# Kernel optimization log

Hardware: AMD Instinct MI355X
Metric: run time of the kernel (lower is better)

The kernel has to match this reference:

```python
import jax, jax.numpy as jnp
import numpy as np

DIM = 2048
N_HEADS = 32
N_KV_HEADS = 8
HEAD_DIM = DIM // N_HEADS
B, T = 2, 2048


def setup_inputs() -> dict:
    key = jax.random.key(0)
    ks = jax.random.split(key, 5)
    std = 0.02
    return {
        "x": jax.random.normal(ks[0], (B, T, DIM), dtype=jnp.float32),
        "wq": jax.random.normal(ks[1], (DIM, DIM), dtype=jnp.float32) * std,
        "wk": jax.random.normal(ks[2], (N_KV_HEADS * HEAD_DIM, DIM), dtype=jnp.float32) * std,
        "wv": jax.random.normal(ks[3], (N_KV_HEADS * HEAD_DIM, DIM), dtype=jnp.float32) * std,
        "wo": jax.random.normal(ks[4], (DIM, DIM), dtype=jnp.float32) * std,
    }


def _rope_tables(seq_len, head_dim, dtype):
    inv_freq = 1.0 / (10000.0 ** (jnp.arange(0, head_dim, 2, dtype=jnp.float32) / head_dim))
    t = jnp.arange(seq_len, dtype=jnp.float32)
    freqs = jnp.einsum("i,j->ij", t, inv_freq)          # [T, hd/2]
    emb = jnp.concatenate([freqs, freqs], axis=-1)       # [T, hd]
    return jnp.cos(emb).astype(dtype), jnp.sin(emb).astype(dtype)


def _rotate_half(x):
    h = x.shape[-1] // 2
    return jnp.concatenate([-x[..., h:], x[..., :h]], axis=-1)


def reference(x, wq, wk, wv, wo):
    Bc, Tc, C = x.shape
    q = (x @ wq.T).reshape(Bc, Tc, N_HEADS, HEAD_DIM).transpose(0, 2, 1, 3)      # [B,H,T,hd]
    k = (x @ wk.T).reshape(Bc, Tc, N_KV_HEADS, HEAD_DIM).transpose(0, 2, 1, 3)   # [B,Hk,T,hd]
    v = (x @ wv.T).reshape(Bc, Tc, N_KV_HEADS, HEAD_DIM).transpose(0, 2, 1, 3)

    cos, sin = _rope_tables(Tc, HEAD_DIM, x.dtype)  # [T,hd] broadcast over B,H
    q = q * cos + _rotate_half(q) * sin
    k = k * cos + _rotate_half(k) * sin

    rep = N_HEADS // N_KV_HEADS
    k = jnp.repeat(k, rep, axis=1)  # [B,H,T,hd]
    v = jnp.repeat(v, rep, axis=1)

    scale = 1.0 / np.sqrt(HEAD_DIM)
    scores = jnp.einsum("bhqd,bhkd->bhqk", q, k) * scale   # [B,H,T,T]
    causal = jnp.triu(jnp.ones((Tc, Tc), dtype=bool), k=1)
    scores = jnp.where(causal, jnp.asarray(-jnp.inf, scores.dtype), scores)
    attn = jax.nn.softmax(scores, axis=-1)
    out = jnp.einsum("bhqk,bhkd->bhqd", attn, v)           # [B,H,T,hd]
    out = out.transpose(0, 2, 1, 3).reshape(Bc, Tc, C)
    return out @ wo.T
```

## Files before the change

kernel.cpp:

```cpp
#include <hip/hip_runtime.h>


typedef unsigned short u16;
typedef __attribute__((ext_vector_type(8))) short bf16x8;
typedef __attribute__((ext_vector_type(4))) float f32x4;
typedef __attribute__((ext_vector_type(4))) unsigned short u16x4;

constexpr int T_SEQ = 2048;
constexpr int DIMC  = 2048;
constexpr int NHEAD = 32;
constexpr int HDIM  = 64;
constexpr int KVDIM = 512;
constexpr int BATCH = 2;

__device__ __forceinline__ u16 f2bf(float f) {
    union { float f; unsigned int i; } v; v.f = f;
    unsigned int r = v.i + 0x7FFFu + ((v.i >> 16) & 1u);
    return (u16)(r >> 16);
}
__device__ __forceinline__ u16 f2bf_trunc(float f) {
    union { float f; unsigned int i; } v; v.f = f;
    return (u16)(v.i >> 16);
}

typedef __attribute__((address_space(1))) unsigned int as1_uint;
typedef __attribute__((address_space(3))) unsigned int as3_uint;
__device__ __forceinline__ void glds16(const u16* g, u16* l) {
    __builtin_amdgcn_global_load_lds((as1_uint*)(u16*)g, (as3_uint*)l, 16, 0, 0);
}

__global__ __launch_bounds__(256) void cvt5(const float* __restrict__ x,
                                            const float* __restrict__ wq,
                                            const float* __restrict__ wk,
                                            const float* __restrict__ wv,
                                            const float* __restrict__ wo,
                                            u16* __restrict__ xb,  u16* __restrict__ wqb,
                                            u16* __restrict__ wkb, u16* __restrict__ wvb,
                                            u16* __restrict__ wob) {
    constexpr int E0 = BATCH * T_SEQ * DIMC;
    constexpr int E1 = E0 + DIMC * DIMC;
    constexpr int E2 = E1 + KVDIM * DIMC;
    constexpr int E3 = E2 + KVDIM * DIMC;
    constexpr int E4 = E3 + DIMC * DIMC;
    for (int i = (blockIdx.x * 256 + threadIdx.x) * 4; i < E4; i += gridDim.x * 1024) {
        const float* s; u16* d; int off;
        if (i < E0)      { s = x;  d = xb;  off = 0;  }
        else if (i < E1) { s = wq; d = wqb; off = E0; }
        else if (i < E2) { s = wk; d = wkb; off = E1; }
        else if (i < E3) { s = wv; d = wvb; off = E2; }
        else             { s = wo; d = wob; off = E3; }
        f32x4 v = *(const f32x4*)(s + (i - off));
        u16x4 o;
        #pragma unroll
        for (int e = 0; e < 4; ++e) o[e] = f2bf(v[e]);
        *(u16x4*)(d + (i - off)) = o;
    }
}

template <bool OUTF32>
__device__ __forceinline__ void gemm_core(const u16* __restrict__ A,
                                          const u16* __restrict__ W,
                                          void* __restrict__ Cv,
                                          int rowBase, int colBase,
                                          int N, int K, bool rope) {
    __shared__ __align__(16) u16 As[2 * 128 * 32];
    __shared__ __align__(16) u16 Bs[2 * 128 * 32];

    const int tid  = threadIdx.x;
    const int lane = tid & 63;
    const int w    = tid >> 6;
    const int quad = lane >> 4;
    const int ln   = lane & 15;
    const int wm = (w >> 1) * 64;
    const int wn = (w & 1) * 64;

    f32x4 acc[4][4] = {};

    const int srow = lane >> 2;
    const int scol = (lane & 3) * 8;
    const u16* aC0 = A + (size_t)(rowBase + w * 16 + srow) * K + scol;
    const u16* aC1 = A + (size_t)(rowBase + (w + 4) * 16 + srow) * K + scol;
    const u16* bC0 = W + (size_t)(colBase + w * 16 + srow) * K + scol;
    const u16* bC1 = W + (size_t)(colBase + (w + 4) * 16 + srow) * K + scol;
    u16* asl0 = As + w * 512;
    u16* asl1 = As + (w + 4) * 512;
    u16* bsl0 = Bs + w * 512;
    u16* bsl1 = Bs + (w + 4) * 512;

    for (int kk = 0; kk < K; kk += 64) {
        __syncthreads();
        glds16(aC0 + kk, asl0);
        glds16(aC1 + kk, asl1);
        glds16(bC0 + kk, bsl0);
        glds16(bC1 + kk, bsl1);
        glds16(aC0 + kk + 32, asl0 + 4096);
        glds16(aC1 + kk + 32, asl1 + 4096);
        glds16(bC0 + kk + 32, bsl0 + 4096);
        glds16(bC1 + kk + 32, bsl1 + 4096);
        __syncthreads();

        #pragma unroll
        for (int hp = 0; hp < 2; ++hp) {
            const u16* Ap = As + hp * 4096;
            const u16* Bp = Bs + hp * 4096;
            bf16x8 bw[4];
            #pragma unroll
            for (int j = 0; j < 4; ++j)
                bw[j] = *(const bf16x8*)(Bp + (wn + j * 16 + ln) * 32 + quad * 8);
            #pragma unroll
            for (int i = 0; i < 4; ++i) {
                bf16x8 af = *(const bf16x8*)(Ap + (wm + i * 16 + ln) * 32 + quad * 8);
                #pragma unroll
                for (int j = 0; j < 4; ++j)
                    acc[i][j] = __builtin_amdgcn_mfma_f32_16x16x32_bf16(af, bw[j], acc[i][j], 0, 0, 0);
            }
        }
    }

    if (rope) {
        #pragma unroll
        for (int j = 0; j < 2; ++j) {
            const int d = j * 16 + ln;
            const float invrev = exp2f(-(float)d * (13.287712379549449f / 32.0f))
                                 * 0.15915494309189535f;
            #pragma unroll
            for (int i = 0; i < 4; ++i) {
                #pragma unroll
                for (int r = 0; r < 4; ++r) {
                    const int t = (rowBase + wm + i * 16 + quad * 4 + r) & (T_SEQ - 1);
                    float rev = (float)t * invrev;
                    float fr = rev - floorf(rev);
                    float sn = __builtin_amdgcn_sinf(fr);
                    float cs = __builtin_amdgcn_cosf(fr);
                    float a0 = acc[i][j][r], a2 = acc[i][j + 2][r];
                    acc[i][j][r]     = a0 * cs - a2 * sn;
                    acc[i][j + 2][r] = a2 * cs + a0 * sn;
                }
            }
        }
    }

    #pragma unroll
    for (int i = 0; i < 4; ++i) {
        int mrow = rowBase + wm + i * 16 + quad * 4;
        #pragma unroll
        for (int j = 0; j < 4; ++j) {
            int n = colBase + wn + j * 16 + ln;
            #pragma unroll
            for (int r = 0; r < 4; ++r) {
                if constexpr (OUTF32)
                    ((float*)Cv)[(size_t)(mrow + r) * N + n] = acc[i][j][r];
                else
                    ((u16*)Cv)[(size_t)(mrow + r) * N + n] = f2bf(acc[i][j][r]);
            }
        }
    }
}

__global__ __launch_bounds__(256, 4) void qkv_gemm(const u16* __restrict__ xb,
                                                   const u16* __restrict__ wqb,
                                                   const u16* __restrict__ wkb,
                                                   const u16* __restrict__ wvb,
                                                   u16* __restrict__ Qb,
                                                   u16* __restrict__ Kb,
                                                   u16* __restrict__ Vb) {
    const int nb = blockIdx.x;
    const int rowBase = blockIdx.y * 128;
    const u16* W; u16* C; int colBase, N; bool rope;
    if (nb < 16)      { W = wqb; C = Qb; colBase = nb * 128;        N = DIMC;  rope = true; }
    else if (nb < 20) { W = wkb; C = Kb; colBase = (nb - 16) * 128; N = KVDIM; rope = true; }
    else              { W = wvb; C = Vb; colBase = (nb - 20) * 128; N = KVDIM; rope = false; }
    gemm_core<false>(xb, W, C, rowBase, colBase, N, DIMC, rope);
}

__global__ __launch_bounds__(256, 4) void gemm_out64(const u16* __restrict__ A,
                                                     const u16* __restrict__ W,
                                                     float* __restrict__ C) {
    __shared__ __align__(16) u16 As[2 * 128 * 32];
    __shared__ __align__(16) u16 Bs[2 * 64 * 32];

    const int tid  = threadIdx.x;
    const int lane = tid & 63;
    const int w    = tid >> 6;
    const int quad = lane >> 4;
    const int ln   = lane & 15;
    const int rowBase = blockIdx.y * 128;
    const int colBase = blockIdx.x * 64;
    const int wm = w * 32;
    constexpr int K = DIMC, N = DIMC;

    f32x4 acc[2][4] = {};

    const int srow = lane >> 2;
    const int scol = (lane & 3) * 8;
    const u16* aC0 = A + (size_t)(rowBase + w * 16 + srow) * K + scol;
    const u16* aC1 = A + (size_t)(rowBase + (w + 4) * 16 + srow) * K + scol;
    const u16* bC  = W + (size_t)(colBase + w * 16 + srow) * K + scol;
    u16* asl0 = As + w * 512;
    u16* asl1 = As + (w + 4) * 512;
    u16* bsl  = Bs + w * 512;

    for (int kk = 0; kk < K; kk += 64) {
        __syncthreads();
        glds16(aC0 + kk, asl0);
        glds16(aC1 + kk, asl1);
        glds16(bC  + kk, bsl);
        glds16(aC0 + kk + 32, asl0 + 4096);
        glds16(aC1 + kk + 32, asl1 + 4096);
        glds16(bC  + kk + 32, bsl + 2048);
        __syncthreads();

        #pragma unroll
        for (int hp = 0; hp < 2; ++hp) {
            const u16* Ap = As + hp * 4096;
            const u16* Bp = Bs + hp * 2048;
            bf16x8 bw[4];
            #pragma unroll
            for (int j = 0; j < 4; ++j)
                bw[j] = *(const bf16x8*)(Bp + (j * 16 + ln) * 32 + quad * 8);
            #pragma unroll
            for (int i = 0; i < 2; ++i) {
                bf16x8 af = *(const bf16x8*)(Ap + (wm + i * 16 + ln) * 32 + quad * 8);
                #pragma unroll
                for (int j = 0; j < 4; ++j)
                    acc[i][j] = __builtin_amdgcn_mfma_f32_16x16x32_bf16(af, bw[j], acc[i][j], 0, 0, 0);
            }
        }
    }

    #pragma unroll
    for (int i = 0; i < 2; ++i) {
        int mrow = rowBase + wm + i * 16 + quad * 4;
        #pragma unroll
        for (int j = 0; j < 4; ++j) {
            int n = colBase + j * 16 + ln;
            #pragma unroll
            for (int r = 0; r < 4; ++r)
                C[(size_t)(mrow + r) * N + n] = acc[i][j][r];
        }
    }
}

__global__ __launch_bounds__(256) void transpose_v(const u16* __restrict__ V,
                                                   u16* __restrict__ Vt) {
    __shared__ __align__(16) u16 tile[32][33];
    const int x = threadIdx.x & 31;
    const int y = threadIdx.x >> 5;
    const int tok0 = blockIdx.y * 32;
    const int c0   = blockIdx.x * 32;
    #pragma unroll
    for (int yy = 0; yy < 32; yy += 8)
        tile[y + yy][x] = V[(size_t)(tok0 + y + yy) * KVDIM + c0 + x];
    __syncthreads();
    const int b  = tok0 >> 11;
    const int t0 = tok0 & (T_SEQ - 1);
    #pragma unroll
    for (int yy = 0; yy < 32; yy += 8)
        Vt[(size_t)(b * KVDIM + c0 + y + yy) * T_SEQ + t0 + x] = tile[x][y + yy];
}

__global__ __launch_bounds__(256) void attn(const u16* __restrict__ Q,
                                            const u16* __restrict__ Kx,
                                            const u16* __restrict__ Vt,
                                            u16* __restrict__ O) {
    __shared__ __align__(16) u16 Ks[64][72];
    __shared__ __align__(16) u16 Vs[64][72];
    __shared__ __align__(16) u16 Ps[4][16][72];

    const int tid  = threadIdx.x;
    const int lane = tid & 63;
    const int w    = tid >> 6;
    const int quad = lane >> 4;
    const int ln   = lane & 15;
    const int h    = blockIdx.y;
    const int b    = blockIdx.z;
    const int kvh  = h >> 2;

    const int srow = tid >> 2;
    const int scol = (tid & 3) * 16;
    const u16* kbase = Kx + (size_t)(b * T_SEQ + srow) * KVDIM + kvh * HDIM + scol;
    const u16* vbase = Vt + (size_t)(b * KVDIM + kvh * HDIM + srow) * T_SEQ;

    const float K1 = 0.125f * 1.4426950408889634f;
    const float K2 = 8.0f * 1.4426950408889634f;

    #pragma unroll
    for (int phase = 0; phase < 2; ++phase) {
        const int qt = phase ? (31 - (int)blockIdx.x) : (int)blockIdx.x;
        const int qr0 = qt * 64 + w * 16;

        const u16* qp = Q + (size_t)(b * T_SEQ + qr0 + ln) * DIMC + h * HDIM + quad * 8;
        const bf16x8 aq0 = *(const bf16x8*)qp;
        const bf16x8 aq1 = *(const bf16x8*)(qp + 32);

        f32x4 o[4] = {};
        float lpart[4] = {};

        for (int kt = 0; kt <= qt; ++kt) {
            const int k0 = kt * 64;
            __syncthreads();
            *(bf16x8*)&Ks[srow][scol]     = *(const bf16x8*)(kbase + (size_t)k0 * KVDIM);
            *(bf16x8*)&Ks[srow][scol + 8] = *(const bf16x8*)(kbase + (size_t)k0 * KVDIM + 8);
            *(bf16x8*)&Vs[srow][scol]     = *(const bf16x8*)(vbase + k0 + scol);
            *(bf16x8*)&Vs[srow][scol + 8] = *(const bf16x8*)(vbase + k0 + scol + 8);
            __syncthreads();

            f32x4 s[4];
            #pragma unroll
            for (int st = 0; st < 4; ++st) {
                f32x4 z = {};
                s[st] = __builtin_amdgcn_mfma_f32_16x16x32_bf16(
                            aq0, *(const bf16x8*)&Ks[st * 16 + ln][quad * 8], z, 0, 0, 0);
                s[st] = __builtin_amdgcn_mfma_f32_16x16x32_bf16(
                            aq1, *(const bf16x8*)&Ks[st * 16 + ln][32 + quad * 8], s[st], 0, 0, 0);
            }

            if (kt != qt) {
                #pragma unroll
                for (int r = 0; r < 4; ++r) {
                    float e[4], rs = 0.0f;
                    #pragma unroll
                    for (int st = 0; st < 4; ++st) {
                        e[st] = exp2f(fmaf(s[st][r], K1, -K2));
                        rs += e[st];
                    }
                    lpart[r] += rs;
                    #pragma unroll
                    for (int st = 0; st < 4; ++st)
                        Ps[w][quad * 4 + r][st * 16 + ln] = f2bf_trunc(e[st]);
                }
            } else {
                #pragma unroll
                for (int r = 0; r < 4; ++r) {
                    const int thr = w * 16 + quad * 4 + r;
                    float e[4], rs = 0.0f;
                    #pragma unroll
                    for (int st = 0; st < 4; ++st) {
                        bool masked = (st * 16 + ln > thr);
                        e[st] = masked ? 0.0f : exp2f(fmaf(s[st][r], K1, -K2));
                        rs += e[st];
                    }
                    lpart[r] += rs;
                    #pragma unroll
                    for (int st = 0; st < 4; ++st)
                        Ps[w][quad * 4 + r][st * 16 + ln] = f2bf_trunc(e[st]);
                }
            }
            __asm__ __volatile__("s_waitcnt lgkmcnt(0)" ::: "memory");

            bf16x8 pa0 = *(const bf16x8*)&Ps[w][ln][quad * 8];
            bf16x8 pa1 = *(const bf16x8*)&Ps[w][ln][32 + quad * 8];
            #pragma unroll
            for (int t = 0; t < 4; ++t) {
                o[t] = __builtin_amdgcn_mfma_f32_16x16x32_bf16(
                           pa0, *(const bf16x8*)&Vs[t * 16 + ln][quad * 8], o[t], 0, 0, 0);
                o[t] = __builtin_amdgcn_mfma_f32_16x16x32_bf16(
                           pa1, *(const bf16x8*)&Vs[t * 16 + ln][32 + quad * 8], o[t], 0, 0, 0);
            }
        }

        #pragma unroll
        for (int r = 0; r < 4; ++r) {
            float rs = lpart[r];
            rs += __shfl_xor(rs, 1);
            rs += __shfl_xor(rs, 2);
            rs += __shfl_xor(rs, 4);
            rs += __shfl_xor(rs, 8);
            float inv = 1.0f / rs;
            size_t obase = (size_t)(b * T_SEQ + qr0 + quad * 4 + r) * DIMC + h * HDIM;
            #pragma unroll
            for (int t = 0; t < 4; ++t)
                O[obase + t * 16 + ln] = f2bf(o[t][r] * inv);
        }
    }
}

extern "C" void kernel_launch(void* const* d_in, const int* in_sizes, int n_in,
                              void* d_out, int out_size, void* d_ws, size_t ws_size,
                              hipStream_t stream) {
    const float* x  = (const float*)d_in[0];
    const float* wq = (const float*)d_in[1];
    const float* wk = (const float*)d_in[2];
    const float* wv = (const float*)d_in[3];
    const float* wo = (const float*)d_in[4];
    float* out = (float*)d_out;

    char* ws = (char*)d_ws;
    constexpr size_t MB = 1024 * 1024;
    u16* Qb  = (u16*)(ws);
    u16* Kb  = (u16*)(ws + 16 * MB);
    u16* Vb  = (u16*)(ws + 20 * MB);
    u16* Vtb = (u16*)(ws + 24 * MB);
    u16* AOb = (u16*)(ws + 28 * MB);
    u16* xb  = AOb;
    u16* wqb = (u16*)(ws + 44 * MB);
    u16* wkb = (u16*)(ws + 52 * MB);
    u16* wvb = (u16*)(ws + 54 * MB);
    u16* wob = (u16*)(ws + 56 * MB);
    const int M = BATCH * T_SEQ;

    hipLaunchKernelGGL(cvt5, dim3(2048), dim3(256), 0, stream,
                       x, wq, wk, wv, wo, xb, wqb, wkb, wvb, wob);
    hipLaunchKernelGGL(qkv_gemm, dim3(24, M / 128), dim3(256), 0, stream,
                       xb, wqb, wkb, wvb, Qb, Kb, Vb);
    hipLaunchKernelGGL(transpose_v, dim3(KVDIM / 32, M / 32), dim3(256), 0, stream, Vb, Vtb);
    hipLaunchKernelGGL(attn, dim3(16, NHEAD, BATCH), dim3(256), 0, stream,
                       Qb, Kb, Vtb, AOb);
    hipLaunchKernelGGL(gemm_out64, dim3(DIMC / 64, M / 128), dim3(256), 0, stream,
                       AOb, wob, out);
}
```

Before: 319.7 us.

## Keep softmax probabilities in registers by transposing S MFMA and permuting V layout

Swaps the MFMA operand order so S is computed transposed, which lets each lane hold the probabilities it needs as the A operand of the PV MFMA. The probabilities are packed straight to bf16 pairs in registers instead of going through an LDS round-trip. The V tile is stored in shared memory with a permuted column order so the key indexing matches the register-resident P layout. The row-sum reduction changes to cross-quad shuffles. This removes the LDS writes and reads, the waitcnt stall and the shared P buffer, at the cost of more complex indexing and narrower 8-byte V stores.

```diff
diff --git a/kernel.cpp b/kernel.cpp
--- a/kernel.cpp
+++ b/kernel.cpp
@@ -18,9 +18,10 @@
     unsigned int r = v.i + 0x7FFFu + ((v.i >> 16) & 1u);
     return (u16)(r >> 16);
 }
-__device__ __forceinline__ u16 f2bf_trunc(float f) {
-    union { float f; unsigned int i; } v; v.f = f;
-    return (u16)(v.i >> 16);
+
+__device__ __forceinline__ unsigned int pack2_bf16(float e0, float e1) {
+    return __builtin_amdgcn_perm(__float_as_uint(e1), __float_as_uint(e0),
+                                 0x07060302u);
 }
 
 typedef __attribute__((address_space(1))) unsigned int as1_uint;
@@ -265,7 +266,6 @@
                                             u16* __restrict__ O) {
     __shared__ __align__(16) u16 Ks[64][72];
     __shared__ __align__(16) u16 Vs[64][72];
-    __shared__ __align__(16) u16 Ps[4][16][72];
 
     const int tid  = threadIdx.x;
     const int lane = tid & 63;
@@ -277,7 +277,9 @@
     const int kvh  = h >> 2;
 
     const int srow = tid >> 2;
-    const int scol = (tid & 3) * 16;
+    const int c    = tid & 3;
+    const int scol = c * 16;
+    const int vsb  = 32 * (c >> 1) + 4 * (c & 1);
     const u16* kbase = Kx + (size_t)(b * T_SEQ + srow) * KVDIM + kvh * HDIM + scol;
     const u16* vbase = Vt + (size_t)(b * KVDIM + kvh * HDIM + srow) * T_SEQ;
 
@@ -290,19 +292,26 @@
         const int qr0 = qt * 64 + w * 16;
 
         const u16* qp = Q + (size_t)(b * T_SEQ + qr0 + ln) * DIMC + h * HDIM + quad * 8;
-        const bf16x8 aq0 = *(const bf16x8*)qp;
-        const bf16x8 aq1 = *(const bf16x8*)(qp + 32);
+        const bf16x8 bq0 = *(const bf16x8*)qp;
+        const bf16x8 bq1 = *(const bf16x8*)(qp + 32);
 
         f32x4 o[4] = {};
-        float lpart[4] = {};
+        float lsum = 0.0f;
 
         for (int kt = 0; kt <= qt; ++kt) {
             const int k0 = kt * 64;
             __syncthreads();
             *(bf16x8*)&Ks[srow][scol]     = *(const bf16x8*)(kbase + (size_t)k0 * KVDIM);
             *(bf16x8*)&Ks[srow][scol + 8] = *(const bf16x8*)(kbase + (size_t)k0 * KVDIM + 8);
-            *(bf16x8*)&Vs[srow][scol]     = *(const bf16x8*)(vbase + k0 + scol);
-            *(bf16x8*)&Vs[srow][scol + 8] = *(const bf16x8*)(vbase + k0 + scol + 8);
+            {
+                union { bf16x8 v; u16x4 h4[2]; } va, vb;
+                va.v = *(const bf16x8*)(vbase + k0 + scol);
+                vb.v = *(const bf16x8*)(vbase + k0 + scol + 8);
+                *(u16x4*)&Vs[srow][vsb]      = va.h4[0];
+                *(u16x4*)&Vs[srow][vsb + 8]  = va.h4[1];
+                *(u16x4*)&Vs[srow][vsb + 16] = vb.h4[0];
+                *(u16x4*)&Vs[srow][vsb + 24] = vb.h4[1];
+            }
             __syncthreads();
 
             f32x4 s[4];
@@ -310,63 +319,58 @@
             for (int st = 0; st < 4; ++st) {
                 f32x4 z = {};
                 s[st] = __builtin_amdgcn_mfma_f32_16x16x32_bf16(
-                            aq0, *(const bf16x8*)&Ks[st * 16 + ln][quad * 8], z, 0, 0, 0);
+                            *(const bf16x8*)&Ks[st * 16 + ln][quad * 8], bq0, z, 0, 0, 0);
                 s[st] = __builtin_amdgcn_mfma_f32_16x16x32_bf16(
-                            aq1, *(const bf16x8*)&Ks[st * 16 + ln][32 + quad * 8], s[st], 0, 0, 0);
-            }
-
+                            *(const bf16x8*)&Ks[st * 16 + ln][32 + quad * 8], bq1, s[st], 0, 0, 0);
+            }
+
+            unsigned int pk[8];
             if (kt != qt) {
                 #pragma unroll
-                for (int r = 0; r < 4; ++r) {
-                    float e[4], rs = 0.0f;
-                    #pragma unroll
-                    for (int st = 0; st < 4; ++st) {
-                        e[st] = exp2f(fmaf(s[st][r], K1, -K2));
-                        rs += e[st];
-                    }
-                    lpart[r] += rs;
-                    #pragma unroll
-                    for (int st = 0; st < 4; ++st)
-                        Ps[w][quad * 4 + r][st * 16 + ln] = f2bf_trunc(e[st]);
+                for (int st = 0; st < 4; ++st) {
+                    float e0 = exp2f(fmaf(s[st][0], K1, -K2));
+                    float e1 = exp2f(fmaf(s[st][1], K1, -K2));
+                    float e2 = exp2f(fmaf(s[st][2], K1, -K2));
+                    float e3 = exp2f(fmaf(s[st][3], K1, -K2));
+                    lsum += (e0 + e1) + (e2 + e3);
+                    pk[2 * st]     = pack2_bf16(e0, e1);
+                    pk[2 * st + 1] = pack2_bf16(e2, e3);
                 }
             } else {
+                const int thr = w * 16 + ln;
                 #pragma unroll
-                for (int r = 0; r < 4; ++r) {
-                    const int thr = w * 16 + quad * 4 + r;
-                    float e[4], rs = 0.0f;
+                for (int st = 0; st < 4; ++st) {
+                    float e[4];
                     #pragma unroll
-                    for (int st = 0; st < 4; ++st) {
-                        bool masked = (st * 16 + ln > thr);
-                        e[st] = masked ? 0.0f : exp2f(fmaf(s[st][r], K1, -K2));
-                        rs += e[st];
+                    for (int r = 0; r < 4; ++r) {
+                        const int key = st * 16 + quad * 4 + r;
+                        e[r] = (key > thr) ? 0.0f : exp2f(fmaf(s[st][r], K1, -K2));
                     }
-                    lpart[r] += rs;
-                    #pragma unroll
-                    for (int st = 0; st < 4; ++st)
-                        Ps[w][quad * 4 + r][st * 16 + ln] = f2bf_trunc(e[st]);
+                    lsum += (e[0] + e[1]) + (e[2] + e[3]);
+                    pk[2 * st]     = pack2_bf16(e[0], e[1]);
+                    pk[2 * st + 1] = pack2_bf16(e[2], e[3]);
                 }
             }
-            __asm__ __volatile__("s_waitcnt lgkmcnt(0)" ::: "memory");
-
-            bf16x8 pa0 = *(const bf16x8*)&Ps[w][ln][quad * 8];
-            bf16x8 pa1 = *(const bf16x8*)&Ps[w][ln][32 + quad * 8];
+
+            union { unsigned int u[4]; bf16x8 v; } a0, a1;
+            a0.u[0] = pk[0]; a0.u[1] = pk[1]; a0.u[2] = pk[2]; a0.u[3] = pk[3];
+            a1.u[0] = pk[4]; a1.u[1] = pk[5]; a1.u[2] = pk[6]; a1.u[3] = pk[7];
+
             #pragma unroll
             for (int t = 0; t < 4; ++t) {
                 o[t] = __builtin_amdgcn_mfma_f32_16x16x32_bf16(
-                           pa0, *(const bf16x8*)&Vs[t * 16 + ln][quad * 8], o[t], 0, 0, 0);
+                           a0.v, *(const bf16x8*)&Vs[t * 16 + ln][quad * 8], o[t], 0, 0, 0);
                 o[t] = __builtin_amdgcn_mfma_f32_16x16x32_bf16(
-                           pa1, *(const bf16x8*)&Vs[t * 16 + ln][32 + quad * 8], o[t], 0, 0, 0);
-            }
-        }
-
+                           a1.v, *(const bf16x8*)&Vs[t * 16 + ln][32 + quad * 8], o[t], 0, 0, 0);
+            }
+        }
+
+        float ls = lsum;
+        ls += __shfl_xor(ls, 16);
+        ls += __shfl_xor(ls, 32);
         #pragma unroll
         for (int r = 0; r < 4; ++r) {
-            float rs = lpart[r];
-            rs += __shfl_xor(rs, 1);
-            rs += __shfl_xor(rs, 2);
-            rs += __shfl_xor(rs, 4);
-            rs += __shfl_xor(rs, 8);
-            float inv = 1.0f / rs;
+            const float inv = 1.0f / __shfl(ls, quad * 4 + r);
             size_t obase = (size_t)(b * T_SEQ + qr0 + quad * 4 + r) * DIMC + h * HDIM;
             #pragma unroll
             for (int t = 0; t < 4; ++t)
```

New measurement: 316.7 us. Within noise of the previous version (-0.9%).
